# Kernel tuning notes

Hardware: AMD Instinct MI355X
Metric: run time of the kernel (lower is better)

Reference implementation:

```python
import jax, jax.numpy as jnp
import numpy as np

N = 100000
E = 1600000
F_IN, F_HID, F_OUT = 128, 64, 1


def setup_inputs() -> dict:
    key = jax.random.key(0)
    ks = jax.random.split(key, 8)
    x = jax.random.normal(ks[0], (N, F_IN), dtype=jnp.float32)
    edge_index = jax.random.randint(ks[1], (2, E), 0, N, dtype=jnp.int64)
    def glorot(k, fan_in, fan_out):
        scale = jnp.sqrt(2.0 / (fan_in + fan_out)).astype(jnp.float32)
        return jax.random.normal(k, (fan_in, fan_out), dtype=jnp.float32) * scale
    W1 = glorot(ks[2], F_IN, F_HID); b1 = jnp.zeros((F_HID,), jnp.float32)
    W2 = glorot(ks[3], F_HID, F_HID); b2 = jnp.zeros((F_HID,), jnp.float32)
    W3 = glorot(ks[4], F_HID, F_OUT); b3 = jnp.zeros((F_OUT,), jnp.float32)
    return {"x": x, "W1": W1, "b1": b1, "W2": W2, "b2": b2, "W3": W3, "b3": b3, "edge_index": edge_index}


def _gcn_norm(edge_index, n):
    # add self-loops, symmetric D^{-1/2} (A+I) D^{-1/2} normalization (PyG GCNConv default)
    loop = jnp.arange(n, dtype=edge_index.dtype)
    src = jnp.concatenate([edge_index[0], loop])
    dst = jnp.concatenate([edge_index[1], loop])
    deg = jax.ops.segment_sum(jnp.ones_like(src, dtype=jnp.float32), dst, num_segments=n)
    dis = jnp.where(deg > 0, jax.lax.rsqrt(jnp.maximum(deg, 1.0)), 0.0)
    norm = dis[src] * dis[dst]  # [E+N]
    return src, dst, norm


def _gcn_conv(h, W, b, src, dst, norm, n):
    h = h @ W                                   # [N, f_out]
    msg = h[src] * norm[:, None]                # gather + scale, [E+N, f_out]
    out = jax.ops.segment_sum(msg, dst, num_segments=n)  # scatter-add
    return out + b


def reference(x, W1, b1, W2, b2, W3, b3, edge_index):
    n = x.shape[0]
    src, dst, norm = _gcn_norm(edge_index, n)
    h = jax.nn.relu(_gcn_conv(x, W1, b1, src, dst, norm, n))
    h = jax.nn.relu(_gcn_conv(h, W2, b2, src, dst, norm, n))
    h = _gcn_conv(h, W3, b3, src, dst, norm, n)
    return jax.nn.sigmoid(h)
```

## Files before the change

kernel.cpp:

```cpp
#include <hip/hip_runtime.h>
#include <math.h>

#define NN 100000
#define NE 1600000
#define NSHARD 4
#define SHARD_W (NN / NSHARD)
#define NCHUNK 64
#define CHUNK_E (NE / NCHUNK)
#define CHUNK_I4 (CHUNK_E / 4)

typedef __attribute__((ext_vector_type(8))) short bf16x8;
typedef __attribute__((ext_vector_type(4))) float f32x4;

__device__ inline unsigned f2bf(float f) {
    unsigned u = __float_as_uint(f);
    u += 0x7FFFu + ((u >> 16) & 1u);
    return u >> 16;
}
__device__ inline float bflo(unsigned v) { return __uint_as_float(v << 16); }
__device__ inline float bfhi(unsigned v) { return __uint_as_float(v & 0xFFFF0000u); }

__global__ __launch_bounds__(256) void k_cnt(const int4* __restrict__ dst4,
                                             unsigned char* __restrict__ cnt,
                                             unsigned char* __restrict__ lrank) {
    __shared__ __align__(16) unsigned ldeg[SHARD_W];
    int t = threadIdx.x;
    int shard = blockIdx.x & (NSHARD - 1);
    int b = blockIdx.x >> 2;
    int lo = shard * SHARD_W;
    for (int i = t; i < SHARD_W; i += 256) ldeg[i] = 0u;
    __syncthreads();
    const int4* p = dst4 + b * CHUNK_I4;
    unsigned char* lr = lrank + b * CHUNK_E;
#pragma unroll 4
    for (int j = t; j < CHUNK_I4; j += 256) {
        int4 d = p[j];
        unsigned ex = (unsigned)(d.x - lo);
        unsigned ey = (unsigned)(d.y - lo);
        unsigned ez = (unsigned)(d.z - lo);
        unsigned ew = (unsigned)(d.w - lo);
        if (ex < SHARD_W) lr[4 * j + 0] = (unsigned char)atomicAdd(&ldeg[ex], 1u);
        if (ey < SHARD_W) lr[4 * j + 1] = (unsigned char)atomicAdd(&ldeg[ey], 1u);
        if (ez < SHARD_W) lr[4 * j + 2] = (unsigned char)atomicAdd(&ldeg[ez], 1u);
        if (ew < SHARD_W) lr[4 * j + 3] = (unsigned char)atomicAdd(&ldeg[ew], 1u);
    }
    __syncthreads();
    unsigned* cb32 = (unsigned*)cnt + b * (NN / 4) + shard * (SHARD_W / 4);
    for (int i = t; i < SHARD_W / 4; i += 256) {
        uint4 v = *(const uint4*)&ldeg[4 * i];
        cb32[i] = (v.x & 255u) | ((v.y & 255u) << 8) | ((v.z & 255u) << 16)
                | ((v.w & 255u) << 24);
    }
}

__global__ __launch_bounds__(256) void k_blkscan(unsigned* __restrict__ cnt32,
                                                 int4* __restrict__ deg4) {
    int i = blockIdx.x * 256 + threadIdx.x;
    if (i >= NN / 4) return;
    unsigned c[NCHUNK];
#pragma unroll
    for (int b = 0; b < NCHUNK; ++b) c[b] = cnt32[b * (NN / 4) + i];
    unsigned a0 = 0, a1 = 0, a2 = 0, a3 = 0;
#pragma unroll
    for (int b = 0; b < NCHUNK; ++b) {
        unsigned v = c[b];
        cnt32[b * (NN / 4) + i] = a0 | (a1 << 8) | (a2 << 16) | (a3 << 24);
        a0 += v & 255u;
        a1 += (v >> 8) & 255u;
        a2 += (v >> 16) & 255u;
        a3 += v >> 24;
    }
    deg4[i] = make_int4((int)a0, (int)a1, (int)a2, (int)a3);
}

__global__ void k_bsum(const int* __restrict__ deg, int* __restrict__ bsums) {
    __shared__ int s[256];
    int t = threadIdx.x;
    int i = blockIdx.x * 256 + t;
    s[t] = (i < NN) ? deg[i] : 0;
    __syncthreads();
    for (int off = 128; off > 0; off >>= 1) {
        if (t < off) s[t] += s[t + off];
        __syncthreads();
    }
    if (t == 0) bsums[blockIdx.x] = s[0];
}

__global__ void k_scan512(const int* __restrict__ bsums, int* __restrict__ bscan) {
    __shared__ int s[512];
    int t = threadIdx.x;
    int v = (t < 391) ? bsums[t] : 0;
    s[t] = v;
    __syncthreads();
    for (int off = 1; off < 512; off <<= 1) {
        int x = (t >= off) ? s[t - off] : 0;
        __syncthreads();
        s[t] += x;
        __syncthreads();
    }
    bscan[t] = s[t] - v;
}

__global__ void k_rowptr(const int* __restrict__ deg, const int* __restrict__ bscan,
                         int* __restrict__ rowptr, float* __restrict__ dis) {
    __shared__ int s[256];
    int t = threadIdx.x;
    int i = blockIdx.x * 256 + t;
    int d = (i < NN) ? deg[i] : 0;
    s[t] = d;
    __syncthreads();
    for (int off = 1; off < 256; off <<= 1) {
        int x = (t >= off) ? s[t - off] : 0;
        __syncthreads();
        s[t] += x;
        __syncthreads();
    }
    if (i < NN) {
        int rp = bscan[blockIdx.x] + s[t] - d;
        rowptr[i] = rp;
        dis[i] = rsqrtf((float)(d + 1));
    }
    if (i == 0) rowptr[NN] = NE;
}

__global__ __launch_bounds__(256) void k_build_csr(
    const int4* __restrict__ src4, const int4* __restrict__ dst4,
    const unsigned char* __restrict__ blkoff, const unsigned* __restrict__ lr4,
    const int* __restrict__ rowptr, int* __restrict__ csr) {
    int shard = blockIdx.x & (NSHARD - 1);
    int bsh = blockIdx.x >> 2;
    int stride = (gridDim.x >> 2) * 256;
    int lo = shard * SHARD_W;
    const int NE4 = NE / 4;
    for (int i = bsh * 256 + threadIdx.x; i < NE4; i += stride) {
        int4 d = dst4[i];
        int4 s = src4[i];
        unsigned lr = lr4[i];
        const unsigned char* off = blkoff + (i / CHUNK_I4) * NN;
        unsigned ex = (unsigned)(d.x - lo);
        unsigned ey = (unsigned)(d.y - lo);
        unsigned ez = (unsigned)(d.z - lo);
        unsigned ew = (unsigned)(d.w - lo);
        if (ex < SHARD_W) csr[rowptr[d.x] + off[d.x] + (lr & 255u)] = s.x;
        if (ey < SHARD_W) csr[rowptr[d.y] + off[d.y] + ((lr >> 8) & 255u)] = s.y;
        if (ez < SHARD_W) csr[rowptr[d.z] + off[d.z] + ((lr >> 16) & 255u)] = s.z;
        if (ew < SHARD_W) csr[rowptr[d.w] + off[d.w] + (lr >> 24)] = s.w;
    }
}

#define XS_LD 136
__global__ __launch_bounds__(256) void k_gemm1(
    const float* __restrict__ x, const float* __restrict__ W,
    const float* __restrict__ dis, unsigned short* __restrict__ tsb) {
    __shared__ unsigned short xs[64 * XS_LD];
    __shared__ unsigned short wt[64 * XS_LD];
    int t = threadIdx.x;
    int row0 = blockIdx.x * 64;
    for (int i = t; i < 64 * 64; i += 256) {
        int n = i & 63, k2 = i >> 6;
        float w0 = W[(2 * k2) * 64 + n];
        float w1 = W[(2 * k2 + 1) * 64 + n];
        *(unsigned*)&wt[n * XS_LD + 2 * k2] = f2bf(w0) | (f2bf(w1) << 16);
    }
    for (int i = t; i < 64 * 32; i += 256) {
        int r = i >> 5, c4 = i & 31;
        int gr = row0 + r;
        uint2 p = {0u, 0u};
        if (gr < NN) {
            float4 v = *(const float4*)&x[gr * 128 + 4 * c4];
            p.x = f2bf(v.x) | (f2bf(v.y) << 16);
            p.y = f2bf(v.z) | (f2bf(v.w) << 16);
        }
        *(uint2*)&xs[r * XS_LD + 4 * c4] = p;
    }
    __syncthreads();
    int w = t >> 6, l = t & 63;
    int lm = l & 15, lg = l >> 4;
    const unsigned short* ap = &xs[(16 * w + lm) * XS_LD + 8 * lg];
    const unsigned short* bp = &wt[lm * XS_LD + 8 * lg];
    f32x4 acc0 = {0, 0, 0, 0}, acc1 = {0, 0, 0, 0}, acc2 = {0, 0, 0, 0}, acc3 = {0, 0, 0, 0};
#pragma unroll
    for (int kb = 0; kb < 4; ++kb) {
        bf16x8 a  = *(const bf16x8*)(ap + 32 * kb);
        bf16x8 b0 = *(const bf16x8*)(bp + 32 * kb);
        bf16x8 b1 = *(const bf16x8*)(bp + 16 * XS_LD + 32 * kb);
        bf16x8 b2 = *(const bf16x8*)(bp + 32 * XS_LD + 32 * kb);
        bf16x8 b3 = *(const bf16x8*)(bp + 48 * XS_LD + 32 * kb);
        acc0 = __builtin_amdgcn_mfma_f32_16x16x32_bf16(a, b0, acc0, 0, 0, 0);
        acc1 = __builtin_amdgcn_mfma_f32_16x16x32_bf16(a, b1, acc1, 0, 0, 0);
        acc2 = __builtin_amdgcn_mfma_f32_16x16x32_bf16(a, b2, acc2, 0, 0, 0);
        acc3 = __builtin_amdgcn_mfma_f32_16x16x32_bf16(a, b3, acc3, 0, 0, 0);
    }
    int rbase = row0 + 16 * w + 4 * lg;
#pragma unroll
    for (int r = 0; r < 4; ++r) {
        int row = rbase + r;
        if (row < NN) {
            float dv = dis[row];
            unsigned short* o = &tsb[row * 64 + lm];
            o[0]  = (unsigned short)f2bf(acc0[r] * dv);
            o[16] = (unsigned short)f2bf(acc1[r] * dv);
            o[32] = (unsigned short)f2bf(acc2[r] * dv);
            o[48] = (unsigned short)f2bf(acc3[r] * dv);
        }
    }
}

#define HS_LD 72
__global__ __launch_bounds__(256) void k_gemm2(
    const unsigned short* __restrict__ hb, const float* __restrict__ W,
    const float* __restrict__ dis, unsigned short* __restrict__ tsb) {
    __shared__ unsigned short hs[64 * HS_LD];
    __shared__ unsigned short wh[64 * HS_LD];
    __shared__ unsigned short wl[64 * HS_LD];
    int t = threadIdx.x;
    int row0 = blockIdx.x * 64;
    for (int i = t; i < 64 * 32; i += 256) {
        int n = i & 63, k2 = i >> 6;
        float w0 = W[(2 * k2) * 64 + n];
        float w1 = W[(2 * k2 + 1) * 64 + n];
        unsigned h0 = f2bf(w0), h1 = f2bf(w1);
        *(unsigned*)&wh[n * HS_LD + 2 * k2] = h0 | (h1 << 16);
        float r0 = w0 - bflo(h0), r1 = w1 - bflo(h1);
        *(unsigned*)&wl[n * HS_LD + 2 * k2] = f2bf(r0) | (f2bf(r1) << 16);
    }
    const uint4* h4 = (const uint4*)hb;
    for (int i = t; i < 64 * 8; i += 256) {
        int r = i >> 3, c8 = i & 7;
        int gr = row0 + r;
        uint4 v = (gr < NN) ? h4[gr * 8 + c8] : make_uint4(0u, 0u, 0u, 0u);
        *(uint4*)&hs[r * HS_LD + 8 * c8] = v;
    }
    __syncthreads();
    int w = t >> 6, l = t & 63;
    int lm = l & 15, lg = l >> 4;
    const unsigned short* ap = &hs[(16 * w + lm) * HS_LD + 8 * lg];
    const unsigned short* bh = &wh[lm * HS_LD + 8 * lg];
    const unsigned short* bl = &wl[lm * HS_LD + 8 * lg];
    f32x4 acc0 = {0, 0, 0, 0}, acc1 = {0, 0, 0, 0}, acc2 = {0, 0, 0, 0}, acc3 = {0, 0, 0, 0};
#pragma unroll
    for (int kb = 0; kb < 2; ++kb) {
        bf16x8 a  = *(const bf16x8*)(ap + 32 * kb);
        bf16x8 h0 = *(const bf16x8*)(bh + 32 * kb);
        bf16x8 h1 = *(const bf16x8*)(bh + 16 * HS_LD + 32 * kb);
        bf16x8 h2 = *(const bf16x8*)(bh + 32 * HS_LD + 32 * kb);
        bf16x8 h3 = *(const bf16x8*)(bh + 48 * HS_LD + 32 * kb);
        bf16x8 l0 = *(const bf16x8*)(bl + 32 * kb);
        bf16x8 l1 = *(const bf16x8*)(bl + 16 * HS_LD + 32 * kb);
        bf16x8 l2 = *(const bf16x8*)(bl + 32 * HS_LD + 32 * kb);
        bf16x8 l3 = *(const bf16x8*)(bl + 48 * HS_LD + 32 * kb);
        acc0 = __builtin_amdgcn_mfma_f32_16x16x32_bf16(a, h0, acc0, 0, 0, 0);
        acc1 = __builtin_amdgcn_mfma_f32_16x16x32_bf16(a, h1, acc1, 0, 0, 0);
        acc2 = __builtin_amdgcn_mfma_f32_16x16x32_bf16(a, h2, acc2, 0, 0, 0);
        acc3 = __builtin_amdgcn_mfma_f32_16x16x32_bf16(a, h3, acc3, 0, 0, 0);
        acc0 = __builtin_amdgcn_mfma_f32_16x16x32_bf16(a, l0, acc0, 0, 0, 0);
        acc1 = __builtin_amdgcn_mfma_f32_16x16x32_bf16(a, l1, acc1, 0, 0, 0);
        acc2 = __builtin_amdgcn_mfma_f32_16x16x32_bf16(a, l2, acc2, 0, 0, 0);
        acc3 = __builtin_amdgcn_mfma_f32_16x16x32_bf16(a, l3, acc3, 0, 0, 0);
    }
    int rbase = row0 + 16 * w + 4 * lg;
#pragma unroll
    for (int r = 0; r < 4; ++r) {
        int row = rbase + r;
        if (row < NN) {
            float dv = dis[row];
            unsigned short* o = &tsb[row * 64 + lm];
            o[0]  = (unsigned short)f2bf(acc0[r] * dv);
            o[16] = (unsigned short)f2bf(acc1[r] * dv);
            o[32] = (unsigned short)f2bf(acc2[r] * dv);
            o[48] = (unsigned short)f2bf(acc3[r] * dv);
        }
    }
}

__global__ __launch_bounds__(256) void k_agg_relu(
    const unsigned short* __restrict__ tsb, const int* __restrict__ rowptr,
    const int* __restrict__ csr, const float* __restrict__ dis,
    const float* __restrict__ b, unsigned short* __restrict__ hb) {
    int node = blockIdx.x * 4 + (threadIdx.x >> 6);
    if (node >= NN) return;
    int lane = threadIdx.x & 63;
    int oct = lane >> 3;
    int fl = lane & 7;
    const uint4* ts128 = (const uint4*)tsb;
    float a0 = 0.f, a1 = 0.f, a2 = 0.f, a3 = 0.f, a4 = 0.f, a5 = 0.f, a6 = 0.f, a7 = 0.f;
    if (oct == 0) {
        uint4 v = ts128[node * 8 + fl];
        a0 += bflo(v.x); a1 += bfhi(v.x); a2 += bflo(v.y); a3 += bfhi(v.y);
        a4 += bflo(v.z); a5 += bfhi(v.z); a6 += bflo(v.w); a7 += bfhi(v.w);
    }
    int e = rowptr[node] + oct, end = rowptr[node + 1];
    for (; e + 8 < end; e += 16) {
        int s0 = csr[e];
        int s1 = csr[e + 8];
        uint4 v0 = ts128[s0 * 8 + fl];
        uint4 v1 = ts128[s1 * 8 + fl];
        a0 += bflo(v0.x) + bflo(v1.x); a1 += bfhi(v0.x) + bfhi(v1.x);
        a2 += bflo(v0.y) + bflo(v1.y); a3 += bfhi(v0.y) + bfhi(v1.y);
        a4 += bflo(v0.z) + bflo(v1.z); a5 += bfhi(v0.z) + bfhi(v1.z);
        a6 += bflo(v0.w) + bflo(v1.w); a7 += bfhi(v0.w) + bfhi(v1.w);
    }
    if (e < end) {
        uint4 v = ts128[csr[e] * 8 + fl];
        a0 += bflo(v.x); a1 += bfhi(v.x); a2 += bflo(v.y); a3 += bfhi(v.y);
        a4 += bflo(v.z); a5 += bfhi(v.z); a6 += bflo(v.w); a7 += bfhi(v.w);
    }
#pragma unroll
    for (int off = 8; off <= 32; off <<= 1) {
        a0 += __shfl_xor(a0, off); a1 += __shfl_xor(a1, off);
        a2 += __shfl_xor(a2, off); a3 += __shfl_xor(a3, off);
        a4 += __shfl_xor(a4, off); a5 += __shfl_xor(a5, off);
        a6 += __shfl_xor(a6, off); a7 += __shfl_xor(a7, off);
    }
    if (oct == 0) {
        float dv = dis[node];
        float v0 = fmaxf(a0 * dv + b[8 * fl + 0], 0.f);
        float v1 = fmaxf(a1 * dv + b[8 * fl + 1], 0.f);
        float v2 = fmaxf(a2 * dv + b[8 * fl + 2], 0.f);
        float v3 = fmaxf(a3 * dv + b[8 * fl + 3], 0.f);
        float v4 = fmaxf(a4 * dv + b[8 * fl + 4], 0.f);
        float v5 = fmaxf(a5 * dv + b[8 * fl + 5], 0.f);
        float v6 = fmaxf(a6 * dv + b[8 * fl + 6], 0.f);
        float v7 = fmaxf(a7 * dv + b[8 * fl + 7], 0.f);
        uint4 p;
        p.x = f2bf(v0) | (f2bf(v1) << 16);
        p.y = f2bf(v2) | (f2bf(v3) << 16);
        p.z = f2bf(v4) | (f2bf(v5) << 16);
        p.w = f2bf(v6) | (f2bf(v7) << 16);
        ((uint4*)hb)[node * 8 + fl] = p;
    }
}

__global__ void k_gemm3(const unsigned short* __restrict__ hb, const float* __restrict__ W3,
                        const float* __restrict__ dis, float* __restrict__ t3) {
    __shared__ float Ws[64];
    if (threadIdx.x < 64) Ws[threadIdx.x] = W3[threadIdx.x];
    __syncthreads();
    int row = blockIdx.x * 256 + threadIdx.x;
    if (row >= NN) return;
    const uint4* hp = (const uint4*)(hb + row * 64);
    float acc = 0.f;
#pragma unroll
    for (int k = 0; k < 8; ++k) {
        uint4 v = hp[k];
        acc += bflo(v.x) * Ws[8 * k + 0] + bfhi(v.x) * Ws[8 * k + 1]
             + bflo(v.y) * Ws[8 * k + 2] + bfhi(v.y) * Ws[8 * k + 3]
             + bflo(v.z) * Ws[8 * k + 4] + bfhi(v.z) * Ws[8 * k + 5]
             + bflo(v.w) * Ws[8 * k + 6] + bfhi(v.w) * Ws[8 * k + 7];
    }
    t3[row] = acc * dis[row];
}

__global__ void k_out(const float* __restrict__ t3, const int* __restrict__ rowptr,
                      const int* __restrict__ csr, const float* __restrict__ dis,
                      const float* __restrict__ b3, float* __restrict__ out) {
    int i = blockIdx.x * 256 + threadIdx.x;
    if (i >= NN) return;
    float acc = t3[i];
    float acc1 = 0.f, acc2 = 0.f, acc3 = 0.f;
    int e = rowptr[i], end = rowptr[i + 1];
    for (; e + 4 <= end; e += 4) {
        acc += t3[csr[e]];
        acc1 += t3[csr[e + 1]];
        acc2 += t3[csr[e + 2]];
        acc3 += t3[csr[e + 3]];
    }
    for (; e < end; ++e) acc += t3[csr[e]];
    float z = ((acc + acc1) + (acc2 + acc3)) * dis[i] + b3[0];
    out[i] = 1.f / (1.f + __expf(-z));
}

extern "C" void kernel_launch(void* const* d_in, const int* in_sizes, int n_in,
                              void* d_out, int out_size, void* d_ws, size_t ws_size,
                              hipStream_t stream) {
    const float* x  = (const float*)d_in[0];
    const float* W1 = (const float*)d_in[1];
    const float* b1 = (const float*)d_in[2];
    const float* W2 = (const float*)d_in[3];
    const float* b2 = (const float*)d_in[4];
    const float* W3 = (const float*)d_in[5];
    const float* b3 = (const float*)d_in[6];
    const int*   ei = (const int*)d_in[7];
    const int* src = ei;
    const int* dst = ei + NE;
    float* out = (float*)d_out;

    unsigned short* TSB = (unsigned short*)d_ws;
    unsigned short* HB  = TSB + (size_t)NN * 64;
    float* dis    = (float*)(HB + (size_t)NN * 64);
    float* t3     = dis + NN;
    int*   deg    = (int*)(t3 + NN);
    int*   rowptr = deg + NN;
    int*   bsums  = rowptr + NN + 8;
    int*   bscan  = bsums + 512;
    int*   csr    = bscan + 512;
    unsigned char* lrank = (unsigned char*)TSB;
    unsigned char* cnt   = (unsigned char*)HB;

    const int nbN = (NN + 255) / 256;
    const int nbG = (NN + 63) / 64;
    const int nbA = (NN + 3) / 4;

    k_cnt<<<NSHARD * NCHUNK, 256, 0, stream>>>((const int4*)dst, cnt, lrank);
    k_blkscan<<<(NN / 4 + 255) / 256, 256, 0, stream>>>((unsigned*)cnt, (int4*)deg);
    k_bsum<<<nbN, 256, 0, stream>>>(deg, bsums);
    k_scan512<<<1, 512, 0, stream>>>(bsums, bscan);
    k_rowptr<<<nbN, 256, 0, stream>>>(deg, bscan, rowptr, dis);
    k_build_csr<<<2048, 256, 0, stream>>>((const int4*)src, (const int4*)dst,
                                          cnt, (const unsigned*)lrank, rowptr, csr);

    k_gemm1<<<nbG, 256, 0, stream>>>(x, W1, dis, TSB);
    k_agg_relu<<<nbA, 256, 0, stream>>>(TSB, rowptr, csr, dis, b1, HB);

    k_gemm2<<<nbG, 256, 0, stream>>>(HB, W2, dis, TSB);
    k_agg_relu<<<nbA, 256, 0, stream>>>(TSB, rowptr, csr, dis, b2, HB);

    k_gemm3<<<nbN, 256, 0, stream>>>(HB, W3, dis, t3);
    k_out<<<nbN, 256, 0, stream>>>(t3, rowptr, csr, dis, b3, out);
}
```

Baseline: 297.1 us.

## Aggregate edges per 64-node block with balanced edge split and LDS accumulation

Changes the hidden-layer aggregation from one wavefront per node to one block per 64 nodes. The block's contiguous CSR edge range is split evenly across 32 eight-lane groups, and a shared-memory map gives each edge's destination row. Each group accumulates runs of edges that share a destination and flushes them into shared-memory accumulators with atomics. A final pass adds the self-loop term, bias and ReLU. The aim is to balance work across nodes with uneven degree and to cut the per-node wave overhead, at the cost of LDS atomics, a serial per-node map fill, and a fixed 3072-edge map capacity per block.

Measured after the change: 344.7 us. 16.0% more time.

```diff
diff --git a/kernel.cpp b/kernel.cpp
--- a/kernel.cpp
+++ b/kernel.cpp
@@ -273,61 +273,93 @@
     }
 }
 
+#define AGG_NB 64
+#define AGG_LD 68
+#define AGG_MAPCAP 3072
+
+#define AGG_FLUSH()                                                        \
+    if (cur >= 0) {                                                        \
+        float* fp = &sacc[cur * AGG_LD + fl * 8];                          \
+        atomicAdd(&fp[0], a0); atomicAdd(&fp[1], a1);                      \
+        atomicAdd(&fp[2], a2); atomicAdd(&fp[3], a3);                      \
+        atomicAdd(&fp[4], a4); atomicAdd(&fp[5], a5);                      \
+        atomicAdd(&fp[6], a6); atomicAdd(&fp[7], a7);                      \
+        a0 = a1 = a2 = a3 = a4 = a5 = a6 = a7 = 0.f;                       \
+    }
+
+#define AGG_ACC(v)                                                         \
+    a0 += bflo(v.x); a1 += bfhi(v.x); a2 += bflo(v.y); a3 += bfhi(v.y);    \
+    a4 += bflo(v.z); a5 += bfhi(v.z); a6 += bflo(v.w); a7 += bfhi(v.w);
+
 __global__ __launch_bounds__(256) void k_agg_relu(
     const unsigned short* __restrict__ tsb, const int* __restrict__ rowptr,
     const int* __restrict__ csr, const float* __restrict__ dis,
     const float* __restrict__ b, unsigned short* __restrict__ hb) {
-    int node = blockIdx.x * 4 + (threadIdx.x >> 6);
-    if (node >= NN) return;
-    int lane = threadIdx.x & 63;
-    int oct = lane >> 3;
-    int fl = lane & 7;
+    __shared__ float sacc[AGG_NB * AGG_LD];
+    __shared__ unsigned char map8[AGG_MAPCAP];
+    __shared__ float sb[64];
+    int t = threadIdx.x;
+    int n0 = blockIdx.x * AGG_NB;
+    int nb = min(AGG_NB, NN - n0);
+    int ebase = rowptr[n0];
+    int eend = rowptr[n0 + nb];
+    if (t < 64) sb[t] = b[t];
+    for (int i = t; i < AGG_NB * AGG_LD; i += 256) sacc[i] = 0.f;
+    __syncthreads();
+    if (t < nb) {
+        int r0 = rowptr[n0 + t], r1 = rowptr[n0 + t + 1];
+        for (int e = r0; e < r1; ++e) {
+            int idx = e - ebase;
+            if (idx < AGG_MAPCAP) map8[idx] = (unsigned char)t;
+        }
+    }
+    __syncthreads();
+    int grp = t >> 3, fl = t & 7;
+    int Eb = eend - ebase;
+    int C = (Eb + 31) >> 5;
+    int gbeg = ebase + grp * C;
+    int gend = min(gbeg + C, eend);
     const uint4* ts128 = (const uint4*)tsb;
     float a0 = 0.f, a1 = 0.f, a2 = 0.f, a3 = 0.f, a4 = 0.f, a5 = 0.f, a6 = 0.f, a7 = 0.f;
-    if (oct == 0) {
-        uint4 v = ts128[node * 8 + fl];
-        a0 += bflo(v.x); a1 += bfhi(v.x); a2 += bflo(v.y); a3 += bfhi(v.y);
-        a4 += bflo(v.z); a5 += bfhi(v.z); a6 += bflo(v.w); a7 += bfhi(v.w);
-    }
-    int e = rowptr[node] + oct, end = rowptr[node + 1];
-    for (; e + 8 < end; e += 16) {
+    int cur = -1;
+    for (int e = gbeg; e < gend; e += 2) {
         int s0 = csr[e];
-        int s1 = csr[e + 8];
+        int r0 = map8[e - ebase];
+        int e1 = e + 1;
+        bool h1 = e1 < gend;
+        int s1 = h1 ? csr[e1] : s0;
+        int r1 = h1 ? (int)map8[e1 - ebase] : -2;
         uint4 v0 = ts128[s0 * 8 + fl];
         uint4 v1 = ts128[s1 * 8 + fl];
-        a0 += bflo(v0.x) + bflo(v1.x); a1 += bfhi(v0.x) + bfhi(v1.x);
-        a2 += bflo(v0.y) + bflo(v1.y); a3 += bfhi(v0.y) + bfhi(v1.y);
-        a4 += bflo(v0.z) + bflo(v1.z); a5 += bfhi(v0.z) + bfhi(v1.z);
-        a6 += bflo(v0.w) + bflo(v1.w); a7 += bfhi(v0.w) + bfhi(v1.w);
-    }
-    if (e < end) {
-        uint4 v = ts128[csr[e] * 8 + fl];
-        a0 += bflo(v.x); a1 += bfhi(v.x); a2 += bflo(v.y); a3 += bfhi(v.y);
-        a4 += bflo(v.z); a5 += bfhi(v.z); a6 += bflo(v.w); a7 += bfhi(v.w);
-    }
-#pragma unroll
-    for (int off = 8; off <= 32; off <<= 1) {
-        a0 += __shfl_xor(a0, off); a1 += __shfl_xor(a1, off);
-        a2 += __shfl_xor(a2, off); a3 += __shfl_xor(a3, off);
-        a4 += __shfl_xor(a4, off); a5 += __shfl_xor(a5, off);
-        a6 += __shfl_xor(a6, off); a7 += __shfl_xor(a7, off);
-    }
-    if (oct == 0) {
-        float dv = dis[node];
-        float v0 = fmaxf(a0 * dv + b[8 * fl + 0], 0.f);
-        float v1 = fmaxf(a1 * dv + b[8 * fl + 1], 0.f);
-        float v2 = fmaxf(a2 * dv + b[8 * fl + 2], 0.f);
-        float v3 = fmaxf(a3 * dv + b[8 * fl + 3], 0.f);
-        float v4 = fmaxf(a4 * dv + b[8 * fl + 4], 0.f);
-        float v5 = fmaxf(a5 * dv + b[8 * fl + 5], 0.f);
-        float v6 = fmaxf(a6 * dv + b[8 * fl + 6], 0.f);
-        float v7 = fmaxf(a7 * dv + b[8 * fl + 7], 0.f);
+        if (r0 != cur) { AGG_FLUSH(); cur = r0; }
+        AGG_ACC(v0)
+        if (h1) {
+            if (r1 != cur) { AGG_FLUSH(); cur = r1; }
+            AGG_ACC(v1)
+        }
+    }
+    AGG_FLUSH();
+    __syncthreads();
+    for (int i = t; i < nb * 8; i += 256) {
+        int node = i >> 3, oct = i & 7;
+        int gn = n0 + node;
+        const float* ap = &sacc[node * AGG_LD + oct * 8];
+        uint4 sv = ts128[gn * 8 + oct];
+        float dv = dis[gn];
+        float f0 = fmaxf((ap[0] + bflo(sv.x)) * dv + sb[oct * 8 + 0], 0.f);
+        float f1 = fmaxf((ap[1] + bfhi(sv.x)) * dv + sb[oct * 8 + 1], 0.f);
+        float f2 = fmaxf((ap[2] + bflo(sv.y)) * dv + sb[oct * 8 + 2], 0.f);
+        float f3 = fmaxf((ap[3] + bfhi(sv.y)) * dv + sb[oct * 8 + 3], 0.f);
+        float f4 = fmaxf((ap[4] + bflo(sv.z)) * dv + sb[oct * 8 + 4], 0.f);
+        float f5 = fmaxf((ap[5] + bfhi(sv.z)) * dv + sb[oct * 8 + 5], 0.f);
+        float f6 = fmaxf((ap[6] + bflo(sv.w)) * dv + sb[oct * 8 + 6], 0.f);
+        float f7 = fmaxf((ap[7] + bfhi(sv.w)) * dv + sb[oct * 8 + 7], 0.f);
         uint4 p;
-        p.x = f2bf(v0) | (f2bf(v1) << 16);
-        p.y = f2bf(v2) | (f2bf(v3) << 16);
-        p.z = f2bf(v4) | (f2bf(v5) << 16);
-        p.w = f2bf(v6) | (f2bf(v7) << 16);
-        ((uint4*)hb)[node * 8 + fl] = p;
+        p.x = f2bf(f0) | (f2bf(f1) << 16);
+        p.y = f2bf(f2) | (f2bf(f3) << 16);
+        p.z = f2bf(f4) | (f2bf(f5) << 16);
+        p.w = f2bf(f6) | (f2bf(f7) << 16);
+        ((uint4*)hb)[gn * 8 + oct] = p;
     }
 }
 
@@ -399,7 +431,7 @@
 
     const int nbN = (NN + 255) / 256;
     const int nbG = (NN + 63) / 64;
-    const int nbA = (NN + 3) / 4;
+    const int nbAgg = (NN + AGG_NB - 1) / AGG_NB;
 
     k_cnt<<<NSHARD * NCHUNK, 256, 0, stream>>>((const int4*)dst, cnt, lrank);
     k_blkscan<<<(NN / 4 + 255) / 256, 256, 0, stream>>>((unsigned*)cnt, (int4*)deg);
@@ -410,10 +442,10 @@
                                           cnt, (const unsigned*)lrank, rowptr, csr);
 
     k_gemm1<<<nbG, 256, 0, stream>>>(x, W1, dis, TSB);
-    k_agg_relu<<<nbA, 256, 0, stream>>>(TSB, rowptr, csr, dis, b1, HB);
+    k_agg_relu<<<nbAgg, 256, 0, stream>>>(TSB, rowptr, csr, dis, b1, HB);
 
     k_gemm2<<<nbG, 256, 0, stream>>>(HB, W2, dis, TSB);
-    k_agg_relu<<<nbA, 256, 0, stream>>>(TSB, rowptr, csr, dis, b2, HB);
+    k_agg_relu<<<nbAgg, 256, 0, stream>>>(TSB, rowptr, csr, dis, b2, HB);
 
     k_gemm3<<<nbN, 256, 0, stream>>>(HB, W3, dis, t3);
     k_out<<<nbN, 256, 0, stream>>>(t3, rowptr, csr, dis, b3, out);
```
